# Kernel optimization log

Measured on AMD Instinct MI355X. Metric: run time of the kernel, lower is better.

Reference implementation:

```python
import jax, jax.numpy as jnp
import numpy as np

ALIBI_SLOPES = jnp.array([0.6299605249, 0.396850263, 0.25, 0.1574901312,
                          0.0992125657, 0.0625, 0.0393725328, 0.0248031414,
                          0.015625, 0.0098431332, 0.0062007854, 0.00390625],
                         dtype=jnp.float32)
H, D = 12, 64
SCALE = D ** (-0.5)


def setup_inputs() -> dict:
    key = jax.random.key(0)
    ks = jax.random.split(key, 9)
    B, S, E = 4, 2048, 768
    s = 0.02
    return {
        "x": jax.random.normal(ks[0], (B, S, E), dtype=jnp.float32),
        "Wq": jax.random.normal(ks[1], (E, E), dtype=jnp.float32) * s,
        "bq": jnp.zeros((E,), dtype=jnp.float32),
        "Wk": jax.random.normal(ks[2], (E, E), dtype=jnp.float32) * s,
        "bk": jnp.zeros((E,), dtype=jnp.float32),
        "Wv": jax.random.normal(ks[3], (E, E), dtype=jnp.float32) * s,
        "bv": jnp.zeros((E,), dtype=jnp.float32),
        "Wo": jax.random.normal(ks[4], (E, E), dtype=jnp.float32) * s,
        "bo": jnp.zeros((E,), dtype=jnp.float32),
    }


def reference(x, Wq, bq, Wk, bk, Wv, bv, Wo, bo):
    B, S, E = x.shape
    # projections (weights stored input-major: y = x @ W + b)
    q = (x @ Wq + bq).reshape(B, S, H, D).transpose(0, 2, 1, 3)  # [B,H,S,D]
    k = (x @ Wk + bk).reshape(B, S, H, D).transpose(0, 2, 1, 3)
    v = (x @ Wv + bv).reshape(B, S, H, D).transpose(0, 2, 1, 3)

    scores = jnp.einsum('bhqd,bhkd->bhqk', q, k) * SCALE  # [B,H,S,S]

    pos = jnp.arange(S, dtype=jnp.float32)
    a = ALIBI_SLOPES[:, None] * pos[None, :]          # [H,S]
    alibi = a[:, :, None] - a[:, None, :]             # [H,S,S]
    scores = scores + alibi[None]

    causal = jnp.triu(jnp.ones((S, S), dtype=bool), k=1)  # True above diag
    scores = jnp.where(causal[None, None], -jnp.inf, scores)

    attn = jax.nn.softmax(scores, axis=-1)
    o = jnp.einsum('bhqk,bhkd->bhqd', attn, v)  # [B,H,S,D]

    # Faithful to original: view of contiguous (B,H,S,D) buffer as (B,S,E)
    # (head-major flatten, reproducing the original module's reshape).
    o = o.reshape(B, S, E)
    return o @ Wo + bo
```

## Files before the change

### kernel.cpp

```cpp
#include <hip/hip_runtime.h>
#include <hip/hip_bf16.h>
#include <cstdint>
#include <cstddef>

#define B_ 4
#define S_ 2048
#define E_ 768
#define H_ 12
#define D_ 64

typedef __bf16 bf16x8 __attribute__((ext_vector_type(8)));
typedef float f32x4 __attribute__((ext_vector_type(4)));

__constant__ float c_slopes[12] = {
    0.6299605249f, 0.396850263f, 0.25f, 0.1574901312f,
    0.0992125657f, 0.0625f, 0.0393725328f, 0.0248031414f,
    0.015625f, 0.0098431332f, 0.0062007854f, 0.00390625f};

__device__ __forceinline__ unsigned short f2bf_u(float f) {
    unsigned u = __builtin_bit_cast(unsigned, f);
    u += 0x7fffu + ((u >> 16) & 1u);
    return (unsigned short)(u >> 16);
}
__device__ __forceinline__ __bf16 f2bf(float f) {
    unsigned short s = f2bf_u(f);
    return __builtin_bit_cast(__bf16, s);
}

__device__ __forceinline__ void gload_lds16(const void* g, void* l) {
    __builtin_amdgcn_global_load_lds(
        (const __attribute__((address_space(1))) unsigned int*)g,
        (__attribute__((address_space(3))) unsigned int*)l, 16, 0, 0);
}

__global__ __launch_bounds__(256) void cvt_x(const float* __restrict__ src,
                                             __bf16* __restrict__ dst) {
    int i = (blockIdx.x * 256 + threadIdx.x) * 4;
    float4 v = *(const float4*)(src + i);
    ushort4 o;
    o.x = f2bf_u(v.x); o.y = f2bf_u(v.y); o.z = f2bf_u(v.z); o.w = f2bf_u(v.w);
    *(ushort4*)((unsigned short*)dst + i) = o;
}

__global__ __launch_bounds__(256) void wtrans(const float* __restrict__ W0,
                                              const float* __restrict__ W1,
                                              const float* __restrict__ W2,
                                              const float* __restrict__ W3,
                                              __bf16* __restrict__ Wt) {
    const float* W = blockIdx.z == 0 ? W0 : blockIdx.z == 1 ? W1
                   : blockIdx.z == 2 ? W2 : W3;
    __bf16* out = Wt + (size_t)blockIdx.z * E_ * E_;
    __shared__ alignas(16) __bf16 ts[64 * 72];
    const int t = threadIdx.x;
    const int k0 = blockIdx.y * 64, n0 = blockIdx.x * 64;
#pragma unroll
    for (int i = 0; i < 4; i++) {
        int idx = i * 256 + t;
        int row = idx >> 4, c4 = idx & 15;
        float4 v = *(const float4*)(W + (size_t)(k0 + row) * E_ + n0 + c4 * 4);
        ts[(c4 * 4 + 0) * 72 + row] = f2bf(v.x);
        ts[(c4 * 4 + 1) * 72 + row] = f2bf(v.y);
        ts[(c4 * 4 + 2) * 72 + row] = f2bf(v.z);
        ts[(c4 * 4 + 3) * 72 + row] = f2bf(v.w);
    }
    __syncthreads();
#pragma unroll
    for (int i = 0; i < 2; i++) {
        int idx = i * 256 + t;
        int r = idx >> 3, c8 = idx & 7;
        *(uint4*)((unsigned short*)out + (size_t)(n0 + r) * E_ + k0 + c8 * 8) =
            *(const uint4*)((const unsigned short*)ts + r * 72 + c8 * 8);
    }
}

template <bool PERM>
__global__ __launch_bounds__(256) void gemm_bf(
    const __bf16* __restrict__ A, const __bf16* __restrict__ WtAll,
    const float* __restrict__ b0, const float* __restrict__ b1,
    const float* __restrict__ b2,
    float* __restrict__ outF, __bf16* __restrict__ outB_base) {
    constexpr int Kd = E_, N = E_;
    __shared__ alignas(16) __bf16 Asm[128 * 32];
    __shared__ alignas(16) __bf16 Bsm[128 * 32];

    const int t = threadIdx.x;
    const int w = t >> 6, lane = t & 63;
    const int qm = lane & 15, quad = lane >> 4;
    const int m0 = blockIdx.y * 128, n0 = blockIdx.x * 128;
    const int wm = (w >> 1) * 64, wn = (w & 1) * 64;
    const int z = blockIdx.z;
    const __bf16* Wt = WtAll + (size_t)z * Kd * N;
    const float* bias = PERM ? (z == 0 ? b0 : z == 1 ? b1 : b2) : b0;
    __bf16* outB = PERM ? outB_base + (size_t)z * ((size_t)B_ * S_ * E_) : nullptr;

    float bvv[4];
#pragma unroll
    for (int j = 0; j < 4; j++) bvv[j] = bias[n0 + wn + j * 16 + qm];

    const int crow = lane >> 2;
    const int ccol = lane & 3;

    f32x4 acc[4][4] = {};

    for (int k0 = 0; k0 < Kd; k0 += 32) {
#pragma unroll
        for (int cc = 0; cc < 2; cc++) {
            int chunk = w * 2 + cc;
            int row = chunk * 16 + crow;
            gload_lds16((const unsigned short*)A + (size_t)(m0 + row) * Kd + k0 + ccol * 8,
                        Asm + chunk * 512);
            gload_lds16((const unsigned short*)Wt + (size_t)(n0 + row) * Kd + k0 + ccol * 8,
                        Bsm + chunk * 512);
        }
        __syncthreads();

        bf16x8 af[4], bg[4];
#pragma unroll
        for (int i = 0; i < 4; i++)
            af[i] = *(const bf16x8*)(Asm + (wm + i * 16 + qm) * 32 + quad * 8);
#pragma unroll
        for (int j = 0; j < 4; j++)
            bg[j] = *(const bf16x8*)(Bsm + (wn + j * 16 + qm) * 32 + quad * 8);
#pragma unroll
        for (int i = 0; i < 4; i++)
#pragma unroll
            for (int j = 0; j < 4; j++)
                acc[i][j] = __builtin_amdgcn_mfma_f32_16x16x32_bf16(
                    af[i], bg[j], acc[i][j], 0, 0, 0);
        __syncthreads();
    }

#pragma unroll
    for (int i = 0; i < 4; i++) {
#pragma unroll
        for (int j = 0; j < 4; j++) {
            int col = n0 + wn + j * 16 + qm;
            int rowb = m0 + wm + i * 16 + quad * 4;
            if (PERM && z == 2) {
                int b = rowb >> 11, s = rowb & (S_ - 1);
                int h = col >> 6, d = col & (D_ - 1);
                unsigned short pk4[4];
#pragma unroll
                for (int r = 0; r < 4; r++) pk4[r] = f2bf_u(acc[i][j][r] + bvv[j]);
                uint2 pv;
                pv.x = (unsigned)pk4[0] | ((unsigned)pk4[1] << 16);
                pv.y = (unsigned)pk4[2] | ((unsigned)pk4[3] << 16);
                *(uint2*)((unsigned short*)outB +
                          ((size_t)(b * H_ + h) * D_ + d) * S_ + s) = pv;
            } else {
#pragma unroll
                for (int r = 0; r < 4; r++) {
                    int row = rowb + r;
                    float val = acc[i][j][r] + bvv[j];
                    if (PERM) {
                        int b = row >> 11, s = row & (S_ - 1);
                        int h = col >> 6, d = col & (D_ - 1);
                        outB[(((size_t)(b * H_ + h)) * S_ + s) * D_ + d] = f2bf(val);
                    } else {
                        outF[(size_t)row * N + col] = val;
                    }
                }
            }
        }
    }
}

__global__ __launch_bounds__(256, 3) void attn_k(
    const __bf16* __restrict__ Q, const __bf16* __restrict__ K,
    const __bf16* __restrict__ Vt, __bf16* __restrict__ O) {
    __shared__ alignas(16) __bf16 Ksm[2][64 * 32];
    __shared__ alignas(16) __bf16 Vsm[2][64 * 32];
    __shared__ alignas(16) __bf16 Psm[4 * 16 * 64];

    const int t = threadIdx.x;
    const int w = t >> 6, lane = t & 63;
    const int qm = lane & 15, quad = lane >> 4;
    const int xp = blockIdx.y;
    const int qlo = xp, qhi = 31 - xp;
    const int bh = blockIdx.x;
    const float c2 = c_slopes[bh % H_] * 1.44269504f;
    const size_t base = (size_t)bh * S_ * D_;

    const int bbL = qlo * 64 + w * 16;
    const int bbH = qhi * 64 + w * 16;
    const __bf16* qpL = Q + base + (size_t)(bbL + qm) * D_ + quad * 8;
    const __bf16* qpH = Q + base + (size_t)(bbH + qm) * D_ + quad * 8;
    bf16x8 qL0 = *(const bf16x8*)qpL, qL1 = *(const bf16x8*)(qpL + 32);
    bf16x8 qH0 = *(const bf16x8*)qpH, qH1 = *(const bf16x8*)(qpH + 32);

    f32x4 oaccL[4] = {}, oaccH[4] = {};
    float lsumL = 0.f, lsumH = 0.f;
    char* Pb = (char*)Psm + w * 2048;

    const int srow = lane >> 2;
    const int sq = (lane & 3) ^ ((lane >> 3) & 3);
    const unsigned short* Kg = (const unsigned short*)K + base +
                               (size_t)(16 * w + srow) * D_ + sq * 8;
    const unsigned short* Vg = (const unsigned short*)Vt + base +
                               (size_t)(16 * w + srow) * S_ + sq * 8;

    const int cq = (quad ^ ((qm >> 1) & 3)) * 8;
    const int pf = (qm & 7) << 4;

    int kt = 0;

    bf16x8 ak[4][2], bv[4][2];
    auto tilec = [&](const bf16x8& qf0, const bf16x8& qf1, f32x4* oacc,
                     float& lsum, int bb) {
        f32x4 st[4];
#pragma unroll
        for (int i = 0; i < 4; i++) {
            f32x4 zz = {0.f, 0.f, 0.f, 0.f};
            zz = __builtin_amdgcn_mfma_f32_16x16x32_bf16(ak[i][0], qf0, zz, 0, 0, 0);
            zz = __builtin_amdgcn_mfma_f32_16x16x32_bf16(ak[i][1], qf1, zz, 0, 0, 0);
            st[i] = zz;
        }

        const int qi = bb + qm;
        const bool nomask = (kt * 64 + 63) <= bb;
        float ls = 0.f;
        unsigned pk[4][2];
#pragma unroll
        for (int i = 0; i < 4; i++) {
            float bi = -c2 * (float)(kt * 64 + 16 * i + 4 * quad);
            float p[4];
#pragma unroll
            for (int r = 0; r < 4; r++) {
                float tt = st[i][r] * 0.18033688f + (bi - c2 * (float)r);
                float pp = __builtin_amdgcn_exp2f(tt);
                if (!nomask) {
                    int key = kt * 64 + 16 * i + 4 * quad + r;
                    pp = (key > qi) ? 0.f : pp;
                }
                ls += pp;
                p[r] = pp;
            }
            unsigned u0 = __builtin_bit_cast(unsigned, p[0]) + 0x8000u;
            unsigned u1 = __builtin_bit_cast(unsigned, p[1]) + 0x8000u;
            unsigned u2 = __builtin_bit_cast(unsigned, p[2]) + 0x8000u;
            unsigned u3 = __builtin_bit_cast(unsigned, p[3]) + 0x8000u;
            pk[i][0] = __builtin_amdgcn_perm(u1, u0, 0x07060302u);
            pk[i][1] = __builtin_amdgcn_perm(u3, u2, 0x07060302u);
        }
        lsum += ls;

#pragma unroll
        for (int i = 0; i < 4; i++) {
            uint2 pv; pv.x = pk[i][0]; pv.y = pk[i][1];
            *(uint2*)(Pb + qm * 128 + ((32 * i + 8 * quad) ^ pf)) = pv;
        }

        bf16x8 ap0 = *(const bf16x8*)(Pb + qm * 128 + ((quad * 16) ^ pf));
        bf16x8 ap1 = *(const bf16x8*)(Pb + qm * 128 + ((64 + quad * 16) ^ pf));
#pragma unroll
        for (int jd = 0; jd < 4; jd++) {
            oacc[jd] = __builtin_amdgcn_mfma_f32_16x16x32_bf16(
                ap0, bv[jd][0], oacc[jd], 0, 0, 0);
            oacc[jd] = __builtin_amdgcn_mfma_f32_16x16x32_bf16(
                ap1, bv[jd][1], oacc[jd], 0, 0, 0);
        }
    };

    for (kt = 0; kt <= qhi; kt++) {
#pragma unroll
        for (int h = 0; h < 2; h++) {
            gload_lds16(Kg + (size_t)(kt * 64) * D_ + 32 * h, Ksm[h] + w * 512);
            gload_lds16(Vg + kt * 64 + 32 * h, Vsm[h] + w * 512);
        }
        __syncthreads();

#pragma unroll
        for (int i = 0; i < 4; i++) {
            ak[i][0] = *(const bf16x8*)(Ksm[0] + (16 * i + qm) * 32 + cq);
            ak[i][1] = *(const bf16x8*)(Ksm[1] + (16 * i + qm) * 32 + cq);
        }
#pragma unroll
        for (int jd = 0; jd < 4; jd++) {
            bv[jd][0] = *(const bf16x8*)(Vsm[0] + (16 * jd + qm) * 32 + cq);
            bv[jd][1] = *(const bf16x8*)(Vsm[1] + (16 * jd + qm) * 32 + cq);
        }

        tilec(qH0, qH1, oaccH, lsumH, bbH);
        if (kt <= qlo) tilec(qL0, qL1, oaccL, lsumL, bbL);

        __syncthreads();
    }

    auto epi = [&](f32x4* oacc, float lsum, int bb) {
        float lf = lsum;
        lf += __shfl_xor(lf, 16);
        lf += __shfl_xor(lf, 32);
#pragma unroll
        for (int r = 0; r < 4; r++) {
            float lr = __shfl(lf, 4 * quad + r);
            float inv = 1.0f / lr;
            int qrow = bb + 4 * quad + r;
#pragma unroll
            for (int jd = 0; jd < 4; jd++)
                O[base + (size_t)qrow * D_ + 16 * jd + qm] =
                    f2bf(oacc[jd][r] * inv);
        }
    };
    epi(oaccH, lsumH, bbH);
    epi(oaccL, lsumL, bbL);
}

extern "C" void kernel_launch(void* const* d_in, const int* in_sizes, int n_in,
                              void* d_out, int out_size, void* d_ws, size_t ws_size,
                              hipStream_t stream) {
    (void)in_sizes; (void)n_in; (void)out_size; (void)ws_size;
    const float* x  = (const float*)d_in[0];
    const float* Wq = (const float*)d_in[1];
    const float* bq = (const float*)d_in[2];
    const float* Wk = (const float*)d_in[3];
    const float* bk = (const float*)d_in[4];
    const float* Wv = (const float*)d_in[5];
    const float* bv = (const float*)d_in[6];
    const float* Wo = (const float*)d_in[7];
    const float* bo = (const float*)d_in[8];
    float* out = (float*)d_out;

    const size_t n = (size_t)B_ * H_ * S_ * D_;
    __bf16* xb  = (__bf16*)d_ws;
    __bf16* Qb  = xb + n;
    __bf16* Kb  = xb + 2 * n;
    __bf16* Vtb = xb + 3 * n;
    __bf16* Wt  = xb + 4 * n;
    __bf16* Ob  = Qb;

    cvt_x<<<6144, 256, 0, stream>>>(x, xb);
    wtrans<<<dim3(12, 12, 4), 256, 0, stream>>>(Wq, Wk, Wv, Wo, Wt);
    gemm_bf<true><<<dim3(6, 64, 3), 256, 0, stream>>>(
        xb, Wt, bq, bk, bv, nullptr, Qb);
    attn_k<<<dim3(48, 16), 256, 0, stream>>>(Qb, Kb, Vtb, Ob);
    gemm_bf<false><<<dim3(6, 64, 1), 256, 0, stream>>>(
        Ob, Wt + 3 * (size_t)E_ * E_, bo, nullptr, nullptr, out, nullptr);
}
```

Baseline: 248.2 us.

## Double-buffer K/V tiles in LDS to prefetch the next tile during compute

The attention kernel now stages K/V tiles into two LDS buffers. The next tile's global-to-LDS load is issued right after the barrier, so it runs while the current tile's MFMAs and softmax execute, and the trailing barrier of each iteration is gone. The high and low query blocks also get separate P scratch buffers, so their writes and reads no longer share storage. LDS use per block roughly doubles, which could limit how many blocks fit per CU.

```diff
diff --git a/kernel.cpp b/kernel.cpp
--- a/kernel.cpp
+++ b/kernel.cpp
@@ -168,9 +168,10 @@
 __global__ __launch_bounds__(256, 3) void attn_k(
     const __bf16* __restrict__ Q, const __bf16* __restrict__ K,
     const __bf16* __restrict__ Vt, __bf16* __restrict__ O) {
-    __shared__ alignas(16) __bf16 Ksm[2][64 * 32];
-    __shared__ alignas(16) __bf16 Vsm[2][64 * 32];
-    __shared__ alignas(16) __bf16 Psm[4 * 16 * 64];
+    __shared__ alignas(16) __bf16 Ksm[2][2][64 * 32];
+    __shared__ alignas(16) __bf16 Vsm[2][2][64 * 32];
+    __shared__ alignas(16) __bf16 PsmH[4 * 16 * 64];
+    __shared__ alignas(16) __bf16 PsmL[4 * 16 * 64];
 
     const int t = threadIdx.x;
     const int w = t >> 6, lane = t & 63;
@@ -190,7 +191,8 @@
 
     f32x4 oaccL[4] = {}, oaccH[4] = {};
     float lsumL = 0.f, lsumH = 0.f;
-    char* Pb = (char*)Psm + w * 2048;
+    char* PbH = (char*)PsmH + w * 2048;
+    char* PbL = (char*)PsmL + w * 2048;
 
     const int srow = lane >> 2;
     const int sq = (lane & 3) ^ ((lane >> 3) & 3);
@@ -204,9 +206,18 @@
 
     int kt = 0;
 
+    auto stage = [&](int buf, int k) {
+#pragma unroll
+        for (int h = 0; h < 2; h++) {
+            gload_lds16(Kg + (size_t)(k * 64) * D_ + 32 * h,
+                        Ksm[buf][h] + w * 512);
+            gload_lds16(Vg + k * 64 + 32 * h, Vsm[buf][h] + w * 512);
+        }
+    };
+
     bf16x8 ak[4][2], bv[4][2];
     auto tilec = [&](const bf16x8& qf0, const bf16x8& qf1, f32x4* oacc,
-                     float& lsum, int bb) {
+                     float& lsum, int bb, char* Pb) {
         f32x4 st[4];
 #pragma unroll
         for (int i = 0; i < 4; i++) {
@@ -261,29 +272,26 @@
         }
     };
 
+    stage(0, 0);
     for (kt = 0; kt <= qhi; kt++) {
-#pragma unroll
-        for (int h = 0; h < 2; h++) {
-            gload_lds16(Kg + (size_t)(kt * 64) * D_ + 32 * h, Ksm[h] + w * 512);
-            gload_lds16(Vg + kt * 64 + 32 * h, Vsm[h] + w * 512);
-        }
+        const int cur = kt & 1;
         __syncthreads();
 
+        if (kt < qhi) stage(cur ^ 1, kt + 1);
+
 #pragma unroll
         for (int i = 0; i < 4; i++) {
-            ak[i][0] = *(const bf16x8*)(Ksm[0] + (16 * i + qm) * 32 + cq);
-            ak[i][1] = *(const bf16x8*)(Ksm[1] + (16 * i + qm) * 32 + cq);
+            ak[i][0] = *(const bf16x8*)(Ksm[cur][0] + (16 * i + qm) * 32 + cq);
+            ak[i][1] = *(const bf16x8*)(Ksm[cur][1] + (16 * i + qm) * 32 + cq);
         }
 #pragma unroll
         for (int jd = 0; jd < 4; jd++) {
-            bv[jd][0] = *(const bf16x8*)(Vsm[0] + (16 * jd + qm) * 32 + cq);
-            bv[jd][1] = *(const bf16x8*)(Vsm[1] + (16 * jd + qm) * 32 + cq);
-        }
-
-        tilec(qH0, qH1, oaccH, lsumH, bbH);
-        if (kt <= qlo) tilec(qL0, qL1, oaccL, lsumL, bbL);
-
-        __syncthreads();
+            bv[jd][0] = *(const bf16x8*)(Vsm[cur][0] + (16 * jd + qm) * 32 + cq);
+            bv[jd][1] = *(const bf16x8*)(Vsm[cur][1] + (16 * jd + qm) * 32 + cq);
+        }
+
+        tilec(qH0, qH1, oaccH, lsumH, bbH, PbH);
+        if (kt <= qlo) tilec(qL0, qL1, oaccL, lsumL, bbL, PbL);
     }
 
     auto epi = [&](f32x4* oacc, float lsum, int bb) {
```

Result: slower. 260.9 us (+5.1%).
